# Performance work log

Measured on AMD Instinct MI355X. Metric: run time of the kernel, lower is better.

Reference implementation:

```python
import jax, jax.numpy as jnp
import numpy as np

# Dims (match init_kwargs): N=81 driving series (perfect square -> zero padding path),
# M=64 encoder LSTM units, P=64 decoder LSTM units, T=128 timesteps, pred_len=1.
N, M, P, T, PRED = 81, 64, 64, 128, 1
SQ = 9                # sqrt(N): mtrx_row = mtrx_col = square_size = 9
C = SQ - 2 + 1        # conv_output_size = square_size - CNN_kernel + 1 = 8
B = 512


def _lstm_cell(x, h, c, Wih, Whh, bih, bhh):
    # torch.nn.LSTMCell: gates order i, f, g, o
    g = x @ Wih.T + bih + h @ Whh.T + bhh
    i, f, gg, o = jnp.split(g, 4, axis=1)
    c = jax.nn.sigmoid(f) * c + jax.nn.sigmoid(i) * jnp.tanh(gg)
    h = jax.nn.sigmoid(o) * jnp.tanh(c)
    return h, c


def setup_inputs():
    key = jax.random.key(0)
    ks = jax.random.split(key, 26)
    def rn(i, shape, s=0.1):
        return jax.random.normal(ks[i], shape, dtype=jnp.float32) * s
    return {
        'X_history': jax.random.normal(ks[0], (B, T, N), dtype=jnp.float32),
        'y_history': jax.random.normal(ks[1], (B, T, 1), dtype=jnp.float32),
        'conv_w': rn(2, (M, 1, 2, SQ)), 'conv_b': rn(3, (M,)),
        'We_w': rn(4, (T, 2 * M)), 'We_b': rn(5, (T,)),
        'Ue_w': rn(6, (T, C)),
        've_w': rn(7, (1, T)),
        'enc_Wih': rn(8, (4 * M, C)), 'enc_Whh': rn(9, (4 * M, M)),
        'enc_bih': rn(10, (4 * M,)), 'enc_bhh': rn(11, (4 * M,)),
        'Wd_w': rn(12, (M, 2 * P)), 'Wd_b': rn(13, (M,)),
        'Ud_w': rn(14, (M, M)),
        'vd_w': rn(15, (1, M)),
        'wt_w': rn(16, (1, M + 1)), 'wt_b': rn(17, (1,)),
        'dec_Wih': rn(18, (4 * P, 1)), 'dec_Whh': rn(19, (4 * P, P)),
        'dec_bih': rn(20, (4 * P,)), 'dec_bhh': rn(21, (4 * P,)),
        'Wy_w': rn(22, (P, P + M)), 'Wy_b': rn(23, (P,)),
        'vy_w': rn(24, (PRED, P)), 'vy_b': rn(25, (PRED,)),
    }


def _forward(X_history, y_history, conv_w, conv_b, We_w, We_b, Ue_w, ve_w,
             enc_Wih, enc_Whh, enc_bih, enc_bhh, Wd_w, Wd_b, Ud_w, vd_w,
             wt_w, wt_b, dec_Wih, dec_Whh, dec_bih, dec_bhh, Wy_w, Wy_b, vy_w, vy_b):
    Bv = X_history.shape[0]
    dt = X_history.dtype
    # ---- encoder CNN (state-independent -> hoisted out of the time loop) ----
    # N=81 is a perfect square: c = inputs[:,t,:].reshape(B,1,9,9), no padding.
    imgs = X_history.reshape(Bv, T, SQ, SQ)
    K = conv_w[:, 0]  # (M, 2, SQ); kernel width == image width -> per-row dot product
    conv = (jnp.einsum('btrw,mw->btmr', imgs[:, :, : SQ - 1, :], K[:, 0])
            + jnp.einsum('btrw,mw->btmr', imgs[:, :, 1:, :], K[:, 1])
            + conv_b[None, None, :, None])
    conv = jax.nn.relu(conv)  # (B, T, M, C); dropout is identity in eval

    # ---- encoder: input attention + LSTMCell recurrence over T ----
    def enc_step(carry, c_t):  # c_t: (B, M, C)
        h, s = carry
        x = jnp.concatenate([h, s], axis=1) @ We_w.T + We_b      # (B, T)
        z = jnp.tanh(x[:, None, :] + c_t @ Ue_w.T)               # (B, M, T)
        e = (z @ ve_w.T)[:, :, 0]                                # (B, M)
        alpha = jax.nn.softmax(e, axis=1)
        w_in = jnp.einsum('bm,bmc->bc', alpha, c_t)              # (B, C)
        h, s = _lstm_cell(w_in, h, s, enc_Wih, enc_Whh, enc_bih, enc_bhh)
        return (h, s), h

    h0 = jnp.zeros((Bv, M), dt)
    _, hs = jax.lax.scan(jax.checkpoint(enc_step), (h0, h0), jnp.swapaxes(conv, 0, 1))
    encoded = jnp.swapaxes(hs, 0, 1)  # (B, T, M)

    # ---- decoder: temporal attention + LSTMCell recurrence over T ----
    Uenc = encoded @ Ud_w.T  # loop-invariant U_d(encoded_inputs), (B, T, M)

    def dec_step(carry, y_t):  # y_t: (B, 1)
        d, sp = carry
        x1 = jnp.concatenate([d, sp], axis=1) @ Wd_w.T + Wd_b    # (B, M)
        z1 = jnp.tanh(x1[:, None, :] + Uenc)                     # (B, T, M)
        l = z1 @ vd_w.T                                          # (B, T, 1)
        beta = jax.nn.softmax(l, axis=1)
        c_t = jnp.sum(beta * encoded, axis=1)                    # (B, M)
        y_tilda = jnp.concatenate([c_t, y_t], axis=1) @ wt_w.T + wt_b
        d, sp = _lstm_cell(y_tilda, d, sp, dec_Wih, dec_Whh, dec_bih, dec_bhh)
        return (d, sp), c_t

    d0 = jnp.zeros((Bv, P), dt)
    (d, _), cts = jax.lax.scan(jax.checkpoint(dec_step), (d0, d0), jnp.swapaxes(y_history, 0, 1))
    c_last = cts[-1]
    out = (jnp.concatenate([d, c_last], axis=1) @ Wy_w.T + Wy_b) @ vy_w.T + vy_b
    return out  # (B, pred_len)


def reference(X_history, y_history, conv_w, conv_b, We_w, We_b, Ue_w, ve_w,
              enc_Wih, enc_Whh, enc_bih, enc_bhh, Wd_w, Wd_b, Ud_w, vd_w,
              wt_w, wt_b, dec_Wih, dec_Whh, dec_bih, dec_bhh, Wy_w, Wy_b, vy_w, vy_b):
    return _forward(X_history, y_history, conv_w, conv_b, We_w, We_b, Ue_w, ve_w,
                    enc_Wih, enc_Whh, enc_bih, enc_bhh, Wd_w, Wd_b, Ud_w, vd_w,
                    wt_w, wt_b, dec_Wih, dec_Whh, dec_bih, dec_bhh, Wy_w, Wy_b, vy_w, vy_b)
```

## Files before the change

kernel.cpp:

```cpp
#include <hip/hip_runtime.h>


#define TSTEPS 128
#define HALF   19652

#define ENC    0
#define UENC   8192
#define UE     16896
#define CTLT   17920
#define XVE    18464
#define HSB4   18720
#define GBUF   18864
#define RED    19120
#define IMG    19376
#define LBUF   19460
#define CTV    19588

#define DC_WT    (UE + 64)
#define DC_DWIH  (UE + 192)
#define DC_DBIAS (UE + 448)
#define DC_WDB   (UE + 704)
#define DC_WYB   (UE + 768)
#define DC_VY    (UE + 832)
#define DC_SC    (UE + 896)
#define DC_YH    CTLT
#define GB2      RED
#define TYP      IMG
#define REDS     LBUF

__device__ __forceinline__ float rcpf(float x) { return __builtin_amdgcn_rcpf(x); }
__device__ __forceinline__ float fsigm(float x) { return rcpf(1.0f + __expf(-x)); }
__device__ __forceinline__ float ftanh(float x) { return 1.0f - 2.0f * rcpf(1.0f + __expf(2.0f * x)); }

#define FMA4(d_, p_, q_) \
    d_ = fmaf((p_).x, (q_).x, d_); d_ = fmaf((p_).y, (q_).y, d_); \
    d_ = fmaf((p_).z, (q_).z, d_); d_ = fmaf((p_).w, (q_).w, d_);

__global__ __launch_bounds__(512, 1) void dstp_kernel(
    const float* __restrict__ Xh,   const float* __restrict__ yh,
    const float* __restrict__ convw,const float* __restrict__ convb,
    const float* __restrict__ Wew,  const float* __restrict__ Web,
    const float* __restrict__ Uew,  const float* __restrict__ vew,
    const float* __restrict__ eWih, const float* __restrict__ eWhh,
    const float* __restrict__ ebih, const float* __restrict__ ebhh,
    const float* __restrict__ Wdw,  const float* __restrict__ Wdb,
    const float* __restrict__ Udw,  const float* __restrict__ vdw,
    const float* __restrict__ wtw,  const float* __restrict__ wtb,
    const float* __restrict__ dWih, const float* __restrict__ dWhh,
    const float* __restrict__ dbih, const float* __restrict__ dbhh,
    const float* __restrict__ Wyw,  const float* __restrict__ Wyb,
    const float* __restrict__ vyw,  const float* __restrict__ vyb,
    float* __restrict__ out)
{
    extern __shared__ float smraw[];
    const int tid  = threadIdx.x;
    const int hb   = tid >> 8;
    const int htid = tid & 255;
    const int b    = blockIdx.x * 2 + hb;
    float* S = smraw + hb * HALF;

    for (int i = htid; i < 1024; i += 256) S[UE + i] = Uew[i];
    if (htid < 128) S[XVE + htid * 2 + 1] = vew[htid];
    if (htid < 144) S[HSB4 + htid] = 0.0f;
    __syncthreads();

    for (int t = 0; t < TSTEPS; ++t) {
        if (htid < 81) S[IMG + htid] = Xh[((size_t)b * TSTEPS + t) * 81 + htid];
        {
            int j = htid >> 1, hk = htid & 1;
            const float4* wr  = reinterpret_cast<const float4*>(Wew + j * 128 + hk * 64);
            const float4* hv0 = reinterpret_cast<const float4*>(S + HSB4 + (2 * hk) * 36);
            const float4* hv1 = reinterpret_cast<const float4*>(S + HSB4 + (2 * hk) * 36 + 36);
            float acc = 0.0f;
#pragma unroll
            for (int k = 0; k < 8; ++k) { float4 wv = wr[k],     xv = hv0[k]; FMA4(acc, wv, xv) }
#pragma unroll
            for (int k = 0; k < 8; ++k) { float4 wv = wr[8 + k], xv = hv1[k]; FMA4(acc, wv, xv) }
            acc += __shfl_xor(acc, 1);
            if (hk == 0) S[XVE + j * 2] = acc + Web[j];
        }
        __syncthreads();
#pragma unroll
        for (int rep = 0; rep < 2; ++rep) {
            int idx = htid + rep * 256;
            int m = idx >> 3, r = idx & 7;
            const float* kw = convw + m * 18;
            float acc = convb[m];
#pragma unroll
            for (int w = 0; w < 9; ++w) {
                acc = fmaf(S[IMG + r * 9 + w],     kw[w],     acc);
                acc = fmaf(S[IMG + r * 9 + 9 + w], kw[9 + w], acc);
            }
            S[CTLT + r * 68 + m] = fmaxf(acc, 0.0f);
        }
        __syncthreads();
        const int m = htid & 63;
        float cr[8];
#pragma unroll
        for (int c = 0; c < 8; ++c) cr[c] = S[CTLT + c * 68 + m];
        {
            int w = htid >> 6;
            float eacc = 0.0f;
#pragma unroll 4
            for (int jj = 0; jj < 32; ++jj) {
                int j = w * 32 + jj;
                float4 u0 = *reinterpret_cast<const float4*>(S + UE + j * 8);
                float4 u1 = *reinterpret_cast<const float4*>(S + UE + j * 8 + 4);
                float2 xv = *reinterpret_cast<const float2*>(S + XVE + j * 2);
                float s = xv.x;
                s = fmaf(u0.x, cr[0], s); s = fmaf(u0.y, cr[1], s);
                s = fmaf(u0.z, cr[2], s); s = fmaf(u0.w, cr[3], s);
                s = fmaf(u1.x, cr[4], s); s = fmaf(u1.y, cr[5], s);
                s = fmaf(u1.z, cr[6], s); s = fmaf(u1.w, cr[7], s);
                eacc = fmaf(ftanh(s), xv.y, eacc);
            }
            S[RED + w * 64 + m] = eacc;
        }
        __syncthreads();
        float win[8];
        {
            float e = S[RED + m] + S[RED + 64 + m] + S[RED + 128 + m] + S[RED + 192 + m];
            float mx = e;
#pragma unroll
            for (int dd = 1; dd < 64; dd <<= 1) mx = fmaxf(mx, __shfl_xor(mx, dd));
            float ex = __expf(e - mx);
            float ssum = ex;
#pragma unroll
            for (int dd = 1; dd < 64; dd <<= 1) ssum += __shfl_xor(ssum, dd);
            float al = ex * rcpf(ssum);
#pragma unroll
            for (int c = 0; c < 8; ++c) win[c] = al * cr[c];
#pragma unroll
            for (int dd = 1; dd < 64; dd <<= 1) {
#pragma unroll
                for (int c = 0; c < 8; ++c) win[c] += __shfl_xor(win[c], dd);
            }
        }
        {
            int j = htid;
            const float4* wih = reinterpret_cast<const float4*>(eWih + j * 8);
            float4 a0 = wih[0], a1 = wih[1];
            float acc = ebih[j] + ebhh[j];
            acc = fmaf(a0.x, win[0], acc); acc = fmaf(a0.y, win[1], acc);
            acc = fmaf(a0.z, win[2], acc); acc = fmaf(a0.w, win[3], acc);
            acc = fmaf(a1.x, win[4], acc); acc = fmaf(a1.y, win[5], acc);
            acc = fmaf(a1.z, win[6], acc); acc = fmaf(a1.w, win[7], acc);
            const float4* whh = reinterpret_cast<const float4*>(eWhh + j * 64);
            const float4* hv0 = reinterpret_cast<const float4*>(S + HSB4);
            const float4* hv1 = reinterpret_cast<const float4*>(S + HSB4 + 36);
#pragma unroll
            for (int k = 0; k < 8; ++k) { float4 wv = whh[k],     xv = hv0[k]; FMA4(acc, wv, xv) }
#pragma unroll
            for (int k = 0; k < 8; ++k) { float4 wv = whh[8 + k], xv = hv1[k]; FMA4(acc, wv, xv) }
            S[GBUF + j] = acc;
        }
        __syncthreads();
        if (htid < 64) {
            float gi = S[GBUF + htid],       gf = S[GBUF + 64 + htid];
            float gg = S[GBUF + 128 + htid], go = S[GBUF + 192 + htid];
            int ck = htid >> 5, cl = htid & 31;
            float c = fsigm(gf) * S[HSB4 + (2 + ck) * 36 + cl] + fsigm(gi) * ftanh(gg);
            float h = fsigm(go) * ftanh(c);
            S[HSB4 + ck * 36 + cl] = h;
            S[HSB4 + (2 + ck) * 36 + cl] = c;
            S[ENC + t * 64 + htid] = h;
        }
        __syncthreads();
    }

    if (htid < 65)  S[DC_WT + htid] = wtw[htid];
    if (htid < 256) { S[DC_DWIH + htid] = dWih[htid]; S[DC_DBIAS + htid] = dbih[htid] + dbhh[htid]; }
    if (htid < 64)  { S[DC_WDB + htid] = Wdb[htid]; S[DC_WYB + htid] = Wyb[htid]; S[DC_VY + htid] = vyw[htid]; }
    if (htid < 64)  S[XVE + htid * 2 + 1] = vdw[htid];
    if (htid < 144) S[HSB4 + htid] = 0.0f;
    if (htid < 128) S[DC_YH + htid] = yh[(size_t)b * TSTEPS + htid];
    if (htid == 0)  { S[DC_SC] = wtb[0]; S[DC_SC + 1] = vyb[0]; }
    {
        int j = htid & 63, e8 = htid >> 6;
#pragma unroll 1
        for (int q4 = 0; q4 < 4; ++q4) {
            float acc[8];
#pragma unroll
            for (int i = 0; i < 8; ++i) acc[i] = 0.0f;
#pragma unroll
            for (int kc = 0; kc < 4; ++kc) {
                const float4* ud = reinterpret_cast<const float4*>(Udw + j * 64 + kc * 16);
                float4 u0 = ud[0], u1 = ud[1], u2 = ud[2], u3 = ud[3];
#pragma unroll
                for (int i = 0; i < 8; ++i) {
                    const float4* er = reinterpret_cast<const float4*>(
                        S + ENC + (e8 * 32 + q4 * 8 + i) * 64 + kc * 16);
                    float4 e0 = er[0], e1 = er[1], e2 = er[2], e3 = er[3];
                    float a = acc[i];
                    FMA4(a, u0, e0) FMA4(a, u1, e1) FMA4(a, u2, e2) FMA4(a, u3, e3)
                    acc[i] = a;
                }
            }
#pragma unroll
            for (int i = 0; i < 8; ++i)
                S[UENC + j * 136 + e8 * 32 + q4 * 8 + i] = acc[i];
        }
    }
    __syncthreads();

    for (int t = 0; t < TSTEPS; ++t) {
        {
            int j = htid >> 2, o = htid & 3;
            const float4* wd = reinterpret_cast<const float4*>(Wdw + j * 128 + o * 32);
            const float4* dv = reinterpret_cast<const float4*>(S + HSB4 + o * 36);
            float acc = 0.0f;
#pragma unroll
            for (int k = 0; k < 8; ++k) { float4 wv = wd[k], xv = dv[k]; FMA4(acc, wv, xv) }
            acc += __shfl_xor(acc, 1);
            acc += __shfl_xor(acc, 2);
            if (o == 0) S[XVE + j * 2] = acc + S[DC_WDB + j];
        }
        __syncthreads();
        {
            int tt = htid >> 1, hk = htid & 1;
            float acc = 0.0f;
#pragma unroll 8
            for (int jj = 0; jj < 32; ++jj) {
                int j = hk * 32 + jj;
                float u = S[UENC + j * 136 + tt];
                float2 xv = *reinterpret_cast<const float2*>(S + XVE + j * 2);
                acc = fmaf(ftanh(xv.x + u), xv.y, acc);
            }
            acc += __shfl_xor(acc, 1);
            if (hk == 0) S[LBUF + tt] = acc;
        }
        __syncthreads();
        if (htid < 64) {
            float v0 = S[LBUF + htid], v1 = S[LBUF + 64 + htid];
            float mx = fmaxf(v0, v1);
#pragma unroll
            for (int dd = 1; dd < 64; dd <<= 1) mx = fmaxf(mx, __shfl_xor(mx, dd));
            float e0 = __expf(v0 - mx), e1 = __expf(v1 - mx);
            float s = e0 + e1;
#pragma unroll
            for (int dd = 1; dd < 64; dd <<= 1) s += __shfl_xor(s, dd);
            float r = rcpf(s);
            S[LBUF + htid] = e0 * r;
            S[LBUF + 64 + htid] = e1 * r;
        }
        __syncthreads();
        float hacc = 0.0f;
        {
            const float4* whh = reinterpret_cast<const float4*>(dWhh + htid * 64);
            const float4* dv0 = reinterpret_cast<const float4*>(S + HSB4);
            const float4* dv1 = reinterpret_cast<const float4*>(S + HSB4 + 36);
#pragma unroll
            for (int k = 0; k < 8; ++k) { float4 wv = whh[k],     xv = dv0[k]; FMA4(hacc, wv, xv) }
#pragma unroll
            for (int k = 0; k < 8; ++k) { float4 wv = whh[8 + k], xv = dv1[k]; FMA4(hacc, wv, xv) }
        }
        {
            int j = htid & 63, cc = htid >> 6;
            float acc = 0.0f;
#pragma unroll 8
            for (int i = 0; i < 32; ++i) {
                int ttk = cc * 32 + i;
                acc = fmaf(S[LBUF + ttk], S[ENC + ttk * 64 + j], acc);
            }
            S[GBUF + cc * 64 + j] = acc;
        }
        __syncthreads();
        if (htid < 64) {
            float cv = S[GBUF + htid] + S[GBUF + 64 + htid] +
                       S[GBUF + 128 + htid] + S[GBUF + 192 + htid];
            S[CTV + htid] = cv;
            float p = cv * S[DC_WT + htid];
#pragma unroll
            for (int dd = 1; dd < 64; dd <<= 1) p += __shfl_xor(p, dd);
            if (htid == 0)
                S[REDS] = p + S[DC_YH + t] * S[DC_WT + 64] + S[DC_SC];
        }
        __syncthreads();
        {
            float yt = S[REDS];
            S[GB2 + htid] = hacc + fmaf(yt, S[DC_DWIH + htid], S[DC_DBIAS + htid]);
        }
        __syncthreads();
        if (htid < 64) {
            float gi = S[GB2 + htid],       gf = S[GB2 + 64 + htid];
            float gg = S[GB2 + 128 + htid], go = S[GB2 + 192 + htid];
            int ck = htid >> 5, cl = htid & 31;
            float c = fsigm(gf) * S[HSB4 + (2 + ck) * 36 + cl] + fsigm(gi) * ftanh(gg);
            float dnew = fsigm(go) * ftanh(c);
            S[HSB4 + ck * 36 + cl] = dnew;
            S[HSB4 + (2 + ck) * 36 + cl] = c;
        }
        __syncthreads();
    }

    {
        int p = htid >> 2, o = htid & 3;
        const float4* wy = reinterpret_cast<const float4*>(Wyw + p * 128 + o * 32);
        const float4* sv = reinterpret_cast<const float4*>(
            (o < 2) ? (S + HSB4 + o * 36) : (S + CTV + (o - 2) * 32));
        float acc = 0.0f;
#pragma unroll
        for (int k = 0; k < 8; ++k) { float4 wv = wy[k], xv = sv[k]; FMA4(acc, wv, xv) }
        acc += __shfl_xor(acc, 1);
        acc += __shfl_xor(acc, 2);
        if (o == 0) S[TYP + p] = acc + S[DC_WYB + p];
    }
    __syncthreads();
    if (htid < 64) {
        float v = S[TYP + htid] * S[DC_VY + htid];
#pragma unroll
        for (int dd = 1; dd < 64; dd <<= 1) v += __shfl_xor(v, dd);
        if (htid == 0) out[b] = v + S[DC_SC + 1];
    }
}

extern "C" void kernel_launch(void* const* d_in, const int* in_sizes, int n_in,
                              void* d_out, int out_size, void* d_ws, size_t ws_size,
                              hipStream_t stream) {
    const float* A[26];
    for (int i = 0; i < 26; ++i) A[i] = (const float*)d_in[i];
    (void)in_sizes; (void)n_in; (void)d_ws; (void)ws_size; (void)out_size;

    const int lds_bytes = 2 * HALF * 4;
    (void)hipFuncSetAttribute(reinterpret_cast<const void*>(dstp_kernel),
                              hipFuncAttributeMaxDynamicSharedMemorySize,
                              lds_bytes);

    dstp_kernel<<<dim3(256), dim3(512), lds_bytes, stream>>>(
        A[0], A[1], A[2], A[3], A[4], A[5], A[6], A[7], A[8], A[9],
        A[10], A[11], A[12], A[13], A[14], A[15], A[16], A[17], A[18], A[19],
        A[20], A[21], A[22], A[23], A[24], A[25], (float*)d_out);
}
```

Measured before the change: 1.361 ms.

## Split to one batch per block and cut per-step barriers via double-buffered state

Each workgroup now handles one batch element with 256 threads instead of two elements in 512-thread blocks, so the barriers no longer couple two independent recurrences. Hidden and cell state are double-buffered and the next timestep's image is prefetched, which allows several barriers per step to be removed. LSTM gate rows are interleaved so each quad of lanes holds the i/f/g/o gates for one unit and combines them through shuffles. In the decoder, the Whh matvec moves up to overlap the attention phase. This needs about 80 KB of LDS per block, and with launch bounds of 4 blocks that may limit how many blocks fit on a CU.

```diff
diff --git a/kernel.cpp b/kernel.cpp
--- a/kernel.cpp
+++ b/kernel.cpp
@@ -2,19 +2,19 @@
 
 
 #define TSTEPS 128
-#define HALF   19652
 
 #define ENC    0
 #define UENC   8192
 #define UE     16896
-#define CTLT   17920
-#define XVE    18464
-#define HSB4   18720
-#define GBUF   18864
-#define RED    19120
-#define IMG    19376
-#define LBUF   19460
-#define CTV    19588
+#define EBIAS  17920
+#define CTLT   18176
+#define XVE    18720
+#define HSB    18976
+#define GBUF   19264
+#define RED    19520
+#define IMG    19776
+#define LBUF   19952
+#define SMEMF  20080
 
 #define DC_WT    (UE + 64)
 #define DC_DWIH  (UE + 192)
@@ -24,9 +24,9 @@
 #define DC_VY    (UE + 832)
 #define DC_SC    (UE + 896)
 #define DC_YH    CTLT
-#define GB2      RED
-#define TYP      IMG
-#define REDS     LBUF
+#define BETA     RED
+#define CTV      (RED + 128)
+#define TYP      (RED + 192)
 
 __device__ __forceinline__ float rcpf(float x) { return __builtin_amdgcn_rcpf(x); }
 __device__ __forceinline__ float fsigm(float x) { return rcpf(1.0f + __expf(-x)); }
@@ -36,7 +36,7 @@
     d_ = fmaf((p_).x, (q_).x, d_); d_ = fmaf((p_).y, (q_).y, d_); \
     d_ = fmaf((p_).z, (q_).z, d_); d_ = fmaf((p_).w, (q_).w, d_);
 
-__global__ __launch_bounds__(512, 1) void dstp_kernel(
+__global__ __launch_bounds__(256, 4) void dstp_kernel(
     const float* __restrict__ Xh,   const float* __restrict__ yh,
     const float* __restrict__ convw,const float* __restrict__ convb,
     const float* __restrict__ Wew,  const float* __restrict__ Web,
@@ -52,25 +52,30 @@
     const float* __restrict__ vyw,  const float* __restrict__ vyb,
     float* __restrict__ out)
 {
-    extern __shared__ float smraw[];
-    const int tid  = threadIdx.x;
-    const int hb   = tid >> 8;
-    const int htid = tid & 255;
-    const int b    = blockIdx.x * 2 + hb;
-    float* S = smraw + hb * HALF;
-
-    for (int i = htid; i < 1024; i += 256) S[UE + i] = Uew[i];
-    if (htid < 128) S[XVE + htid * 2 + 1] = vew[htid];
-    if (htid < 144) S[HSB4 + htid] = 0.0f;
+    extern __shared__ float S[];
+    const int tid = threadIdx.x;
+    const int b   = blockIdx.x;
+    const int w   = tid >> 6;
+    const int l   = tid & 63;
+
+    for (int i = tid; i < 1024; i += 256) S[UE + i] = Uew[i];
+    if (tid < 128) S[XVE + tid * 2 + 1] = vew[tid];
+    S[EBIAS + tid] = ebih[tid] + ebhh[tid];
+    S[HSB + tid] = 0.0f;
+    if (tid < 32) S[HSB + 256 + tid] = 0.0f;
+    if (tid < 81) S[IMG + tid] = Xh[((size_t)b * TSTEPS) * 81 + tid];
     __syncthreads();
 
+    int pp = 0;
+
     for (int t = 0; t < TSTEPS; ++t) {
-        if (htid < 81) S[IMG + htid] = Xh[((size_t)b * TSTEPS + t) * 81 + htid];
-        {
-            int j = htid >> 1, hk = htid & 1;
+        if (t + 1 < TSTEPS && tid < 81)
+            S[IMG + ((t + 1) & 1) * 88 + tid] = Xh[((size_t)b * TSTEPS + t + 1) * 81 + tid];
+        {
+            int j = tid >> 1, hk = tid & 1;
             const float4* wr  = reinterpret_cast<const float4*>(Wew + j * 128 + hk * 64);
-            const float4* hv0 = reinterpret_cast<const float4*>(S + HSB4 + (2 * hk) * 36);
-            const float4* hv1 = reinterpret_cast<const float4*>(S + HSB4 + (2 * hk) * 36 + 36);
+            const float4* hv0 = reinterpret_cast<const float4*>(S + HSB + pp * 144 + (2 * hk) * 36);
+            const float4* hv1 = reinterpret_cast<const float4*>(S + HSB + pp * 144 + (2 * hk) * 36 + 36);
             float acc = 0.0f;
 #pragma unroll
             for (int k = 0; k < 8; ++k) { float4 wv = wr[k],     xv = hv0[k]; FMA4(acc, wv, xv) }
@@ -79,27 +84,26 @@
             acc += __shfl_xor(acc, 1);
             if (hk == 0) S[XVE + j * 2] = acc + Web[j];
         }
-        __syncthreads();
 #pragma unroll
         for (int rep = 0; rep < 2; ++rep) {
-            int idx = htid + rep * 256;
+            int idx = tid + rep * 256;
             int m = idx >> 3, r = idx & 7;
             const float* kw = convw + m * 18;
+            const float* ib = S + IMG + (t & 1) * 88 + r * 9;
             float acc = convb[m];
 #pragma unroll
-            for (int w = 0; w < 9; ++w) {
-                acc = fmaf(S[IMG + r * 9 + w],     kw[w],     acc);
-                acc = fmaf(S[IMG + r * 9 + 9 + w], kw[9 + w], acc);
+            for (int wd = 0; wd < 9; ++wd) {
+                acc = fmaf(ib[wd],     kw[wd],     acc);
+                acc = fmaf(ib[9 + wd], kw[9 + wd], acc);
             }
             S[CTLT + r * 68 + m] = fmaxf(acc, 0.0f);
         }
         __syncthreads();
-        const int m = htid & 63;
+
         float cr[8];
 #pragma unroll
-        for (int c = 0; c < 8; ++c) cr[c] = S[CTLT + c * 68 + m];
-        {
-            int w = htid >> 6;
+        for (int c = 0; c < 8; ++c) cr[c] = S[CTLT + c * 68 + l];
+        {
             float eacc = 0.0f;
 #pragma unroll 4
             for (int jj = 0; jj < 32; ++jj) {
@@ -114,12 +118,13 @@
                 s = fmaf(u1.z, cr[6], s); s = fmaf(u1.w, cr[7], s);
                 eacc = fmaf(ftanh(s), xv.y, eacc);
             }
-            S[RED + w * 64 + m] = eacc;
-        }
-        __syncthreads();
+            S[RED + w * 64 + l] = eacc;
+        }
+        __syncthreads();
+
         float win[8];
         {
-            float e = S[RED + m] + S[RED + 64 + m] + S[RED + 128 + m] + S[RED + 192 + m];
+            float e = S[RED + l] + S[RED + 64 + l] + S[RED + 128 + l] + S[RED + 192 + l];
             float mx = e;
 #pragma unroll
             for (int dd = 1; dd < 64; dd <<= 1) mx = fmaxf(mx, __shfl_xor(mx, dd));
@@ -137,46 +142,51 @@
             }
         }
         {
-            int j = htid;
-            const float4* wih = reinterpret_cast<const float4*>(eWih + j * 8);
+            int q = tid & 3, a = tid >> 2;
+            int r = q * 64 + a;
+            const float4* wih = reinterpret_cast<const float4*>(eWih + r * 8);
             float4 a0 = wih[0], a1 = wih[1];
-            float acc = ebih[j] + ebhh[j];
+            float acc = S[EBIAS + r];
             acc = fmaf(a0.x, win[0], acc); acc = fmaf(a0.y, win[1], acc);
             acc = fmaf(a0.z, win[2], acc); acc = fmaf(a0.w, win[3], acc);
             acc = fmaf(a1.x, win[4], acc); acc = fmaf(a1.y, win[5], acc);
             acc = fmaf(a1.z, win[6], acc); acc = fmaf(a1.w, win[7], acc);
-            const float4* whh = reinterpret_cast<const float4*>(eWhh + j * 64);
-            const float4* hv0 = reinterpret_cast<const float4*>(S + HSB4);
-            const float4* hv1 = reinterpret_cast<const float4*>(S + HSB4 + 36);
+            const float4* whh = reinterpret_cast<const float4*>(eWhh + r * 64);
+            const float4* hv0 = reinterpret_cast<const float4*>(S + HSB + pp * 144);
+            const float4* hv1 = reinterpret_cast<const float4*>(S + HSB + pp * 144 + 36);
 #pragma unroll
             for (int k = 0; k < 8; ++k) { float4 wv = whh[k],     xv = hv0[k]; FMA4(acc, wv, xv) }
 #pragma unroll
             for (int k = 0; k < 8; ++k) { float4 wv = whh[8 + k], xv = hv1[k]; FMA4(acc, wv, xv) }
-            S[GBUF + j] = acc;
-        }
-        __syncthreads();
-        if (htid < 64) {
-            float gi = S[GBUF + htid],       gf = S[GBUF + 64 + htid];
-            float gg = S[GBUF + 128 + htid], go = S[GBUF + 192 + htid];
-            int ck = htid >> 5, cl = htid & 31;
-            float c = fsigm(gf) * S[HSB4 + (2 + ck) * 36 + cl] + fsigm(gi) * ftanh(gg);
-            float h = fsigm(go) * ftanh(c);
-            S[HSB4 + ck * 36 + cl] = h;
-            S[HSB4 + (2 + ck) * 36 + cl] = c;
-            S[ENC + t * 64 + htid] = h;
-        }
-        __syncthreads();
-    }
-
-    if (htid < 65)  S[DC_WT + htid] = wtw[htid];
-    if (htid < 256) { S[DC_DWIH + htid] = dWih[htid]; S[DC_DBIAS + htid] = dbih[htid] + dbhh[htid]; }
-    if (htid < 64)  { S[DC_WDB + htid] = Wdb[htid]; S[DC_WYB + htid] = Wyb[htid]; S[DC_VY + htid] = vyw[htid]; }
-    if (htid < 64)  S[XVE + htid * 2 + 1] = vdw[htid];
-    if (htid < 144) S[HSB4 + htid] = 0.0f;
-    if (htid < 128) S[DC_YH + htid] = yh[(size_t)b * TSTEPS + htid];
-    if (htid == 0)  { S[DC_SC] = wtb[0]; S[DC_SC + 1] = vyb[0]; }
+            float actv = (q == 2) ? ftanh(acc) : fsigm(acc);
+            float n1 = __shfl_xor(actv, 1);
+            float n2 = __shfl_xor(actv, 2);
+            float n3 = __shfl_xor(n1, 2);
+            if (q == 0) {
+                int ck = (a >> 5) * 36 + (a & 31);
+                float s_old = S[HSB + pp * 144 + 72 + ck];
+                float cst = n1 * s_old + actv * n2;
+                float h = n3 * ftanh(cst);
+                S[HSB + (pp ^ 1) * 144 + ck] = h;
+                S[HSB + (pp ^ 1) * 144 + 72 + ck] = cst;
+                S[ENC + t * 64 + a] = h;
+            }
+        }
+        __syncthreads();
+        pp ^= 1;
+    }
+
+    if (tid < 65)  S[DC_WT + tid] = wtw[tid];
+    S[DC_DWIH + tid] = dWih[tid];
+    S[DC_DBIAS + tid] = dbih[tid] + dbhh[tid];
+    if (tid < 64)  { S[DC_WDB + tid] = Wdb[tid]; S[DC_WYB + tid] = Wyb[tid]; S[DC_VY + tid] = vyw[tid]; }
+    if (tid < 64)  S[XVE + tid * 2 + 1] = vdw[tid];
+    if (tid < 128) S[DC_YH + tid] = yh[(size_t)b * TSTEPS + tid];
+    S[HSB + tid] = 0.0f;
+    if (tid < 32) S[HSB + 256 + tid] = 0.0f;
+    if (tid == 0)  { S[DC_SC] = wtb[0]; S[DC_SC + 1] = vyb[0]; }
     {
-        int j = htid & 63, e8 = htid >> 6;
+        int e8 = w;
 #pragma unroll 1
         for (int q4 = 0; q4 < 4; ++q4) {
             float acc[8];
@@ -184,7 +194,7 @@
             for (int i = 0; i < 8; ++i) acc[i] = 0.0f;
 #pragma unroll
             for (int kc = 0; kc < 4; ++kc) {
-                const float4* ud = reinterpret_cast<const float4*>(Udw + j * 64 + kc * 16);
+                const float4* ud = reinterpret_cast<const float4*>(Udw + l * 64 + kc * 16);
                 float4 u0 = ud[0], u1 = ud[1], u2 = ud[2], u3 = ud[3];
 #pragma unroll
                 for (int i = 0; i < 8; ++i) {
@@ -198,16 +208,18 @@
             }
 #pragma unroll
             for (int i = 0; i < 8; ++i)
-                S[UENC + j * 136 + e8 * 32 + q4 * 8 + i] = acc[i];
+                S[UENC + l * 136 + e8 * 32 + q4 * 8 + i] = acc[i];
         }
     }
     __syncthreads();
-
+    pp = 0;
+
+    float hacc;
     for (int t = 0; t < TSTEPS; ++t) {
         {
-            int j = htid >> 2, o = htid & 3;
+            int j = tid >> 2, o = tid & 3;
             const float4* wd = reinterpret_cast<const float4*>(Wdw + j * 128 + o * 32);
-            const float4* dv = reinterpret_cast<const float4*>(S + HSB4 + o * 36);
+            const float4* dv = reinterpret_cast<const float4*>(S + HSB + pp * 144 + o * 36);
             float acc = 0.0f;
 #pragma unroll
             for (int k = 0; k < 8; ++k) { float4 wv = wd[k], xv = dv[k]; FMA4(acc, wv, xv) }
@@ -215,9 +227,21 @@
             acc += __shfl_xor(acc, 2);
             if (o == 0) S[XVE + j * 2] = acc + S[DC_WDB + j];
         }
-        __syncthreads();
-        {
-            int tt = htid >> 1, hk = htid & 1;
+        {
+            int r = (tid & 3) * 64 + (tid >> 2);
+            const float4* whh = reinterpret_cast<const float4*>(dWhh + r * 64);
+            const float4* dv0 = reinterpret_cast<const float4*>(S + HSB + pp * 144);
+            const float4* dv1 = reinterpret_cast<const float4*>(S + HSB + pp * 144 + 36);
+            hacc = 0.0f;
+#pragma unroll
+            for (int k = 0; k < 8; ++k) { float4 wv = whh[k],     xv = dv0[k]; FMA4(hacc, wv, xv) }
+#pragma unroll
+            for (int k = 0; k < 8; ++k) { float4 wv = whh[8 + k], xv = dv1[k]; FMA4(hacc, wv, xv) }
+        }
+        __syncthreads();
+
+        {
+            int tt = tid >> 1, hk = tid & 1;
             float acc = 0.0f;
 #pragma unroll 8
             for (int jj = 0; jj < 32; ++jj) {
@@ -230,74 +254,65 @@
             if (hk == 0) S[LBUF + tt] = acc;
         }
         __syncthreads();
-        if (htid < 64) {
-            float v0 = S[LBUF + htid], v1 = S[LBUF + 64 + htid];
+
+        {
+            float v0 = S[LBUF + l], v1 = S[LBUF + 64 + l];
             float mx = fmaxf(v0, v1);
 #pragma unroll
             for (int dd = 1; dd < 64; dd <<= 1) mx = fmaxf(mx, __shfl_xor(mx, dd));
             float e0 = __expf(v0 - mx), e1 = __expf(v1 - mx);
-            float s = e0 + e1;
-#pragma unroll
-            for (int dd = 1; dd < 64; dd <<= 1) s += __shfl_xor(s, dd);
-            float r = rcpf(s);
-            S[LBUF + htid] = e0 * r;
-            S[LBUF + 64 + htid] = e1 * r;
-        }
-        __syncthreads();
-        float hacc = 0.0f;
-        {
-            const float4* whh = reinterpret_cast<const float4*>(dWhh + htid * 64);
-            const float4* dv0 = reinterpret_cast<const float4*>(S + HSB4);
-            const float4* dv1 = reinterpret_cast<const float4*>(S + HSB4 + 36);
-#pragma unroll
-            for (int k = 0; k < 8; ++k) { float4 wv = whh[k],     xv = dv0[k]; FMA4(hacc, wv, xv) }
-#pragma unroll
-            for (int k = 0; k < 8; ++k) { float4 wv = whh[8 + k], xv = dv1[k]; FMA4(hacc, wv, xv) }
-        }
-        {
-            int j = htid & 63, cc = htid >> 6;
+            float ssum = e0 + e1;
+#pragma unroll
+            for (int dd = 1; dd < 64; dd <<= 1) ssum += __shfl_xor(ssum, dd);
+            float rr = rcpf(ssum);
+            if ((l >> 5) == (w & 1)) {
+                if (w < 2) S[BETA + l]      = e0 * rr;
+                else       S[BETA + 64 + l] = e1 * rr;
+            }
+        }
+        {
             float acc = 0.0f;
 #pragma unroll 8
             for (int i = 0; i < 32; ++i) {
-                int ttk = cc * 32 + i;
-                acc = fmaf(S[LBUF + ttk], S[ENC + ttk * 64 + j], acc);
-            }
-            S[GBUF + cc * 64 + j] = acc;
-        }
-        __syncthreads();
-        if (htid < 64) {
-            float cv = S[GBUF + htid] + S[GBUF + 64 + htid] +
-                       S[GBUF + 128 + htid] + S[GBUF + 192 + htid];
-            S[CTV + htid] = cv;
-            float p = cv * S[DC_WT + htid];
+                int ttk = w * 32 + i;
+                acc = fmaf(S[BETA + ttk], S[ENC + ttk * 64 + l], acc);
+            }
+            S[GBUF + w * 64 + l] = acc;
+        }
+        __syncthreads();
+
+        {
+            float cv = S[GBUF + l] + S[GBUF + 64 + l] + S[GBUF + 128 + l] + S[GBUF + 192 + l];
+            if (t == TSTEPS - 1 && w == 0) S[CTV + l] = cv;
+            float p = cv * S[DC_WT + l];
 #pragma unroll
             for (int dd = 1; dd < 64; dd <<= 1) p += __shfl_xor(p, dd);
-            if (htid == 0)
-                S[REDS] = p + S[DC_YH + t] * S[DC_WT + 64] + S[DC_SC];
-        }
-        __syncthreads();
-        {
-            float yt = S[REDS];
-            S[GB2 + htid] = hacc + fmaf(yt, S[DC_DWIH + htid], S[DC_DBIAS + htid]);
-        }
-        __syncthreads();
-        if (htid < 64) {
-            float gi = S[GB2 + htid],       gf = S[GB2 + 64 + htid];
-            float gg = S[GB2 + 128 + htid], go = S[GB2 + 192 + htid];
-            int ck = htid >> 5, cl = htid & 31;
-            float c = fsigm(gf) * S[HSB4 + (2 + ck) * 36 + cl] + fsigm(gi) * ftanh(gg);
-            float dnew = fsigm(go) * ftanh(c);
-            S[HSB4 + ck * 36 + cl] = dnew;
-            S[HSB4 + (2 + ck) * 36 + cl] = c;
-        }
-        __syncthreads();
+            float yt = p + S[DC_YH + t] * S[DC_WT + 64] + S[DC_SC];
+            int q = tid & 3, a = tid >> 2;
+            int r = q * 64 + a;
+            float acc = hacc + fmaf(yt, S[DC_DWIH + r], S[DC_DBIAS + r]);
+            float actv = (q == 2) ? ftanh(acc) : fsigm(acc);
+            float n1 = __shfl_xor(actv, 1);
+            float n2 = __shfl_xor(actv, 2);
+            float n3 = __shfl_xor(n1, 2);
+            if (q == 0) {
+                int ck = (a >> 5) * 36 + (a & 31);
+                float s_old = S[HSB + pp * 144 + 72 + ck];
+                float cst = n1 * s_old + actv * n2;
+                float dnew = n3 * ftanh(cst);
+                S[HSB + (pp ^ 1) * 144 + ck] = dnew;
+                S[HSB + (pp ^ 1) * 144 + 72 + ck] = cst;
+            }
+        }
+        __syncthreads();
+        pp ^= 1;
     }
 
     {
-        int p = htid >> 2, o = htid & 3;
+        int p = tid >> 2, o = tid & 3;
         const float4* wy = reinterpret_cast<const float4*>(Wyw + p * 128 + o * 32);
         const float4* sv = reinterpret_cast<const float4*>(
-            (o < 2) ? (S + HSB4 + o * 36) : (S + CTV + (o - 2) * 32));
+            (o < 2) ? (S + HSB + pp * 144 + o * 36) : (S + CTV + (o - 2) * 32));
         float acc = 0.0f;
 #pragma unroll
         for (int k = 0; k < 8; ++k) { float4 wv = wy[k], xv = sv[k]; FMA4(acc, wv, xv) }
@@ -306,11 +321,11 @@
         if (o == 0) S[TYP + p] = acc + S[DC_WYB + p];
     }
     __syncthreads();
-    if (htid < 64) {
-        float v = S[TYP + htid] * S[DC_VY + htid];
+    if (tid < 64) {
+        float v = S[TYP + tid] * S[DC_VY + tid];
 #pragma unroll
         for (int dd = 1; dd < 64; dd <<= 1) v += __shfl_xor(v, dd);
-        if (htid == 0) out[b] = v + S[DC_SC + 1];
+        if (tid == 0) out[b] = v + S[DC_SC + 1];
     }
 }
 
@@ -321,12 +336,11 @@
     for (int i = 0; i < 26; ++i) A[i] = (const float*)d_in[i];
     (void)in_sizes; (void)n_in; (void)d_ws; (void)ws_size; (void)out_size;
 
-    const int lds_bytes = 2 * HALF * 4;
     (void)hipFuncSetAttribute(reinterpret_cast<const void*>(dstp_kernel),
                               hipFuncAttributeMaxDynamicSharedMemorySize,
-                              lds_bytes);
-
-    dstp_kernel<<<dim3(256), dim3(512), lds_bytes, stream>>>(
+                              SMEMF * 4);
+
+    dstp_kernel<<<dim3(512), dim3(256), SMEMF * 4, stream>>>(
         A[0], A[1], A[2], A[3], A[4], A[5], A[6], A[7], A[8], A[9],
         A[10], A[11], A[12], A[13], A[14], A[15], A[16], A[17], A[18], A[19],
         A[20], A[21], A[22], A[23], A[24], A[25], (float*)d_out);
```

Result: slower. 3.115 ms (+128.9%).
